# Kernel tuning notes

Measured on AMD Instinct MI355X. Metric: run time of the kernel, lower is better.

The kernel has to match this reference:

```python
import jax, jax.numpy as jnp
import numpy as np

N_LAYERS = 4
EPS = 1e-5  # eqx.nn.LayerNorm default


def _kernels(lam, P, B, C, step, L):
    # Annotated-S4 DPLR generating-function kernel (Q = P), vectorized over H channels.
    # lam, P, B, C: (H, N) complex64; step: (H, 1) real. Returns K: (H, L) real.
    omega = jnp.exp((-2j * jnp.pi) * (jnp.arange(L) / L))            # (L,) roots of unity
    g = (2.0 / step) * ((1.0 - omega) / (1.0 + omega))[None, :]      # (H, L) bilinear warp
    c = 2.0 / (1.0 + omega)                                          # (L,)

    def cauchy(v):  # v: (H, N) -> (H, L): sum_n v_n / (g - lambda_n)
        return jnp.sum(v[:, None, :] / (g[:, :, None] - lam[:, None, :]), axis=-1)

    k00 = cauchy(jnp.conj(C) * B)
    k01 = cauchy(jnp.conj(C) * P)
    k10 = cauchy(jnp.conj(P) * B)
    k11 = cauchy(jnp.conj(P) * P)
    at_roots = c[None, :] * (k00 - k01 * (1.0 / (1.0 + k11)) * k10)  # woodbury correction
    return jnp.fft.ifft(at_roots, n=L, axis=-1).real                 # (H, L)


def _causal_conv(u, K):
    # u: (B, L, H) real input, K: (H, L) real kernel -> causal conv along L via zero-padded FFT.
    L = u.shape[1]
    Ud = jnp.fft.rfft(u, n=2 * L, axis=1)                 # (B, F, H)
    Kd = jnp.fft.rfft(K, n=2 * L, axis=-1)                # (H, F)
    return jnp.fft.irfft(Ud * Kd.T[None], n=2 * L, axis=1)[:, :L]


def _forward(x, enc_w, enc_b, dec_w, dec_b, lam_re, lam_im, p_re, p_im, b_re, b_im,
             c_re, c_im, d, log_step, norm_w, norm_b, w1, b1, w2, b2):
    L = x.shape[1]
    h = x @ enc_w.T + enc_b                               # encoder: (B, L, H)
    for i in range(N_LAYERS):
        skip = h
        mu = h.mean(-1, keepdims=True)
        var = ((h - mu) ** 2).mean(-1, keepdims=True)
        hn = (h - mu) / jnp.sqrt(var + EPS) * norm_w[i] + norm_b[i]
        K = _kernels(lam_re[i] + 1j * lam_im[i], p_re[i] + 1j * p_im[i],
                     b_re[i] + 1j * b_im[i], c_re[i] + 1j * c_im[i],
                     jnp.exp(log_step[i])[:, None], L)
        y = _causal_conv(hn, K) + hn * d[i]               # SSM conv + skip-through D term
        y = jax.nn.gelu(y)
        y = (y @ w1[i].T + b1[i]) * jax.nn.sigmoid(y @ w2[i].T + b2[i])  # gated MLP
        h = skip + y
    return h @ dec_w.T + dec_b                            # decoder: (B, L, out)


def setup_inputs() -> dict:
    key = jax.random.key(0)
    B, L, IN, OUT, H, N, NL = 8, 2048, 64, 64, 128, 64, N_LAYERS
    ks = jax.random.split(key, 12)
    rn = lambda k, s, sc: (jax.random.normal(k, s) * sc).astype(jnp.float32)
    return dict(
        x=rn(ks[0], (B, L, IN), 1.0),
        convolve=1,
        enc_w=rn(ks[1], (H, IN), 1.0 / np.sqrt(IN)), enc_b=jnp.zeros((H,), jnp.float32),
        dec_w=rn(ks[2], (OUT, H), 1.0 / np.sqrt(H)), dec_b=jnp.zeros((OUT,), jnp.float32),
        lam_re=-0.5 * jnp.ones((NL, H, N), jnp.float32),  # HiPPO/S4D-style stable poles
        lam_im=jnp.tile(jnp.float32(np.pi) * jnp.arange(N, dtype=jnp.float32), (NL, H, 1)),
        p_re=rn(ks[3], (NL, H, N), 0.5 / np.sqrt(N)), p_im=rn(ks[4], (NL, H, N), 0.5 / np.sqrt(N)),
        b_re=rn(ks[5], (NL, H, N), 1.0), b_im=rn(ks[6], (NL, H, N), 1.0),
        c_re=rn(ks[7], (NL, H, N), 1.0 / np.sqrt(N)), c_im=rn(ks[8], (NL, H, N), 1.0 / np.sqrt(N)),
        d=jnp.ones((NL, H), jnp.float32),
        log_step=(jax.random.uniform(ks[9], (NL, H)) * (np.log(0.1) - np.log(0.001))
                  + np.log(0.001)).astype(jnp.float32),
        norm_w=jnp.ones((NL, H), jnp.float32), norm_b=jnp.zeros((NL, H), jnp.float32),
        w1=rn(ks[10], (NL, H, H), 1.0 / np.sqrt(H)), b1=jnp.zeros((NL, H), jnp.float32),
        w2=rn(ks[11], (NL, H, H), 1.0 / np.sqrt(H)), b2=jnp.zeros((NL, H), jnp.float32),
    )


def reference(x, convolve, enc_w, enc_b, dec_w, dec_b, lam_re, lam_im, p_re, p_im,
              b_re, b_im, c_re, c_im, d, log_step, norm_w, norm_b, w1, b1, w2, b2):
    # convolve is static 1 (True): the FFT-convolution path of the S4 Model.
    return _forward(x, enc_w, enc_b, dec_w, dec_b, lam_re, lam_im, p_re, p_im, b_re, b_im,
                    c_re, c_im, d, log_step, norm_w, norm_b, w1, b1, w2, b2)
```

## Files before the change

kernel.cpp:

```cpp
#include <hip/hip_runtime.h>
#include <hip/hip_bf16.h>


#define Bsz 8
#define Lseq 2048
#define Hdim 128
#define Npol 64
#define NLAYERS 4

typedef __bf16 bf16x8 __attribute__((ext_vector_type(8)));
typedef float f32x16 __attribute__((ext_vector_type(16)));

__device__ __forceinline__ float fast_rcp(float x) { return __builtin_amdgcn_rcpf(x); }
__device__ __forceinline__ float fast_rsq(float x) { return __builtin_amdgcn_rsqf(x); }

__device__ __forceinline__ float2 cmulf(float2 a, float2 b) {
    return make_float2(a.x * b.x - a.y * b.y, a.x * b.y + a.y * b.x);
}
__device__ __forceinline__ float2 cmulc(float2 a, float2 b) {
    return make_float2(a.x * b.x + a.y * b.y, a.y * b.x - a.x * b.y);
}

__device__ __forceinline__ float gelu_f(float v) {
    float z = 0.7978845608028654f * (v + 0.044715f * v * v * v);
    float e = __expf(2.0f * z);
    return v - v * fast_rcp(e + 1.0f);
}

__device__ __forceinline__ int sw(int i) { return (i & ~15) | ((i ^ (i >> 4)) & 15); }

static __device__ const float W16R[8] = {1.f, 0.9238795325f, 0.7071067812f, 0.3826834324f,
                                         0.f, -0.3826834324f, -0.7071067812f, -0.9238795325f};
static __device__ const float W16I[8] = {0.f, -0.3826834324f, -0.7071067812f, -0.9238795325f,
                                         -1.f, -0.9238795325f, -0.7071067812f, -0.3826834324f};
static __device__ const int BR4[16] = {0, 8, 4, 12, 2, 10, 6, 14, 1, 9, 5, 13, 3, 11, 7, 15};
static __device__ const int BR3[8] = {0, 4, 2, 6, 1, 5, 3, 7};

__device__ __forceinline__ float2 twget(const float2* __restrict__ tw, int e) {
    float2 w = tw[e & 2047];
    if (e & 2048) { w.x = -w.x; w.y = -w.y; }
    return w;
}

template <bool INV>
__device__ __forceinline__ void fft16_dif(float2 v[16]) {
#pragma unroll
    for (int mi = 0; mi < 4; mi++) {
        const int m = 8 >> mi;
#pragma unroll
        for (int g = 0; g < 16; g += 2 * m) {
#pragma unroll
            for (int j = 0; j < m; j++) {
                float wr = W16R[j << mi];
                float wi = INV ? -W16I[j << mi] : W16I[j << mi];
                float2 a = v[g + j], b = v[g + j + m];
                float dx = a.x - b.x, dy = a.y - b.y;
                v[g + j] = make_float2(a.x + b.x, a.y + b.y);
                v[g + j + m] = make_float2(dx * wr - dy * wi, dx * wi + dy * wr);
            }
        }
    }
}

template <bool INV>
__device__ __forceinline__ void fft16_dit(float2 v[16]) {
#pragma unroll
    for (int mi = 3; mi >= 0; mi--) {
        const int m = 8 >> mi;
#pragma unroll
        for (int g = 0; g < 16; g += 2 * m) {
#pragma unroll
            for (int j = 0; j < m; j++) {
                float wr = W16R[j << mi];
                float wi = INV ? -W16I[j << mi] : W16I[j << mi];
                float2 a = v[g + j], b = v[g + j + m];
                float bx = b.x * wr - b.y * wi, by = b.x * wi + b.y * wr;
                v[g + j] = make_float2(a.x + bx, a.y + by);
                v[g + j + m] = make_float2(a.x - bx, a.y - by);
            }
        }
    }
}

template <bool INV>
__device__ __forceinline__ void fft8_dif(float2 v[8]) {
#pragma unroll
    for (int mi = 0; mi < 3; mi++) {
        const int m = 4 >> mi;
#pragma unroll
        for (int g = 0; g < 8; g += 2 * m) {
#pragma unroll
            for (int j = 0; j < m; j++) {
                float wr = W16R[j << (mi + 1)];
                float wi = INV ? -W16I[j << (mi + 1)] : W16I[j << (mi + 1)];
                float2 a = v[g + j], b = v[g + j + m];
                float dx = a.x - b.x, dy = a.y - b.y;
                v[g + j] = make_float2(a.x + b.x, a.y + b.y);
                v[g + j + m] = make_float2(dx * wr - dy * wi, dx * wi + dy * wr);
            }
        }
    }
}

__device__ __forceinline__ void fft4096_passA_hz(float2* data, const float2* __restrict__ tw,
                                                 int t, const float2 vin[8]) {
    float2 v[16];
#pragma unroll
    for (int j = 0; j < 8; j++) v[j] = vin[j];
#pragma unroll
    for (int j = 0; j < 8; j++)
        v[j + 8] = cmulf(v[j], make_float2(W16R[j], W16I[j]));
#pragma unroll
    for (int mi = 1; mi < 4; mi++) {
        const int m = 8 >> mi;
#pragma unroll
        for (int g = 0; g < 16; g += 2 * m) {
#pragma unroll
            for (int j = 0; j < m; j++) {
                float wr = W16R[j << mi], wi = W16I[j << mi];
                float2 a = v[g + j], b = v[g + j + m];
                float dx = a.x - b.x, dy = a.y - b.y;
                v[g + j] = make_float2(a.x + b.x, a.y + b.y);
                v[g + j + m] = make_float2(dx * wr - dy * wi, dx * wi + dy * wr);
            }
        }
    }
#pragma unroll
    for (int i = 1; i < 16; i++) v[i] = cmulf(v[i], twget(tw, t * BR4[i]));
#pragma unroll
    for (int i = 0; i < 16; i++) data[sw(i * 256 + t)] = v[i];
}

__device__ __forceinline__ void fft4096_fwd_BC(float2* data, const float2* __restrict__ tw, int t) {
    __syncthreads();
    {
        int j0 = t & 15;
        int base = (t >> 4) * 256 + j0;
        float2 v[16];
#pragma unroll
        for (int k = 0; k < 16; k++) v[k] = data[sw(base + 16 * k)];
        fft16_dif<false>(v);
#pragma unroll
        for (int i = 1; i < 16; i++) v[i] = cmulf(v[i], twget(tw, 16 * j0 * BR4[i]));
#pragma unroll
        for (int i = 0; i < 16; i++) data[sw(base + 16 * i)] = v[i];
    }
    __syncthreads();
    {
        float2 v[16];
#pragma unroll
        for (int k = 0; k < 16; k++) v[k] = data[sw(t * 16 + k)];
        fft16_dif<false>(v);
#pragma unroll
        for (int i = 0; i < 16; i++) data[sw(t * 16 + i)] = v[i];
    }
    __syncthreads();
}

__global__ __launch_bounds__(256, 4) void prep_kernel(const float* __restrict__ lam_re,
                                                      const float* __restrict__ lam_im,
                                                      const float* __restrict__ p_re,
                                                      const float* __restrict__ p_im,
                                                      const float* __restrict__ b_re,
                                                      const float* __restrict__ b_im,
                                                      const float* __restrict__ c_re,
                                                      const float* __restrict__ c_im,
                                                      const float* __restrict__ log_step,
                                                      const float* __restrict__ w1,
                                                      const float* __restrict__ w2,
                                                      float2* __restrict__ tw,
                                                      __bf16* __restrict__ wbf,
                                                      float2* __restrict__ at_roots) {
    int bid = blockIdx.x, t = threadIdx.x;
    if (bid < 8) {
        int k = bid * 256 + t;
        if (k < 2048) {
            double a = -6.283185307179586476925286766559 * (double)k / 4096.0;
            tw[k] = make_float2((float)cos(a), (float)sin(a));
        }
        return;
    }
    if (bid < 264) {
        int i = (bid - 8) * 256 + t;
        int layer = i >> 14, rem = i & 16383;
        wbf[((size_t)layer * 2) * 16384 + rem] = (__bf16)w1[i];
        wbf[((size_t)layer * 2 + 1) * 16384 + rem] = (__bf16)w2[i];
        return;
    }
    int s = bid - 264;
    int h = s & 127, layer = (s >> 7) & 3;
    int l0 = 512 * (s >> 9);
    __shared__ __align__(16) float4 polA[Npol];
    __shared__ __align__(16) float4 polB[Npol];
    __shared__ float n11S[Npol];
    int baseP = (layer * Hdim + h) * Npol;
    if (t < Npol) {
        int n = t;
        float lr = lam_re[baseP + n], li = lam_im[baseP + n];
        float pr = p_re[baseP + n], pi = p_im[baseP + n];
        float br = b_re[baseP + n], bi = b_im[baseP + n];
        float cr = c_re[baseP + n], ci = c_im[baseP + n];
        polA[n] = make_float4(lr, li, cr * br + ci * bi, cr * bi - ci * br);
        polB[n] = make_float4(cr * pr + ci * pi, cr * pi - ci * pr,
                              pr * br + pi * bi, pr * bi - pi * br);
        n11S[n] = pr * pr + pi * pi;
    }
    __syncthreads();
    float step = expf(log_step[layer * Hdim + h]);
    float gs = 2.0f / step;

    float gr[2], gi[2];
#pragma unroll
    for (int j = 0; j < 2; j++) {
        int l = l0 + t + 256 * j;
        float ang = -6.283185307179586f * (float)l / (float)Lseq;
        float wr = cosf(ang), wi = sinf(ang);
        float dr = 1.0f + wr, di = wi;
        float invd2 = fast_rcp(dr * dr + di * di);
        float nr = 1.0f - wr, ni = -wi;
        gr[j] = gs * (nr * dr + ni * di) * invd2;
        gi[j] = gs * (ni * dr - nr * di) * invd2;
    }
    float k00x[2] = {0, 0}, k00y[2] = {0, 0};
    float k01x[2] = {0, 0}, k01y[2] = {0, 0};
    float k10x[2] = {0, 0}, k10y[2] = {0, 0};
    float k11x[2] = {0, 0}, k11y[2] = {0, 0};
#pragma unroll 4
    for (int n = 0; n < Npol; n++) {
        float4 A = polA[n];
        float4 B = polB[n];
        float n11 = n11S[n];
#pragma unroll
        for (int j = 0; j < 2; j++) {
            float er = gr[j] - A.x, ei = gi[j] - A.y;
            float inv2 = fast_rcp(fmaf(er, er, ei * ei));
            float ir = er * inv2;
            float mi = ei * inv2;
            k00x[j] = fmaf(A.z, ir, fmaf(A.w, mi, k00x[j]));
            k00y[j] = fmaf(A.w, ir, fmaf(-A.z, mi, k00y[j]));
            k01x[j] = fmaf(B.x, ir, fmaf(B.y, mi, k01x[j]));
            k01y[j] = fmaf(B.y, ir, fmaf(-B.x, mi, k01y[j]));
            k10x[j] = fmaf(B.z, ir, fmaf(B.w, mi, k10x[j]));
            k10y[j] = fmaf(B.w, ir, fmaf(-B.z, mi, k10y[j]));
            k11x[j] = fmaf(n11, ir, k11x[j]);
            k11y[j] = fmaf(-n11, mi, k11y[j]);
        }
    }
#pragma unroll
    for (int j = 0; j < 2; j++) {
        int l = l0 + t + 256 * j;
        float ang = -6.283185307179586f * (float)l / (float)Lseq;
        float wr = cosf(ang), wi = sinf(ang);
        float dr = 1.0f + wr, di = wi;
        float invd2 = fast_rcp(dr * dr + di * di);
        float cr2 = 2.0f * dr * invd2, ci2 = -2.0f * di * invd2;
        float wr2 = 1.0f + k11x[j], wi2 = k11y[j];
        float w2inv = fast_rcp(fmaf(wr2, wr2, wi2 * wi2));
        float vr = wr2 * w2inv, vi = -wi2 * w2inv;
        float t1x = k01x[j] * k10x[j] - k01y[j] * k10y[j];
        float t1y = k01x[j] * k10y[j] + k01y[j] * k10x[j];
        float t2x = t1x * vr - t1y * vi, t2y = t1x * vi + t1y * vr;
        float ex = k00x[j] - t2x, ey = k00y[j] - t2y;
        at_roots[((size_t)layer * Hdim + h) * Lseq + l] =
            make_float2(cr2 * ex - ci2 * ey, cr2 * ey + ci2 * ex);
    }
}

__global__ __launch_bounds__(256) void kfft_enc_kernel(const float2* __restrict__ at_roots,
                                                       float2* __restrict__ Kd1,
                                                       const float2* __restrict__ tw,
                                                       const float* __restrict__ x,
                                                       const float* __restrict__ enc_w,
                                                       const float* __restrict__ enc_b,
                                                       const float* __restrict__ nw,
                                                       const float* __restrict__ nb,
                                                       float* __restrict__ h,
                                                       float* __restrict__ hnT) {
    __shared__ __align__(16) float smem[11712];
    int bid = blockIdx.x, t = threadIdx.x;
    if (bid < 512) {
        int hh = bid & 127, layer = bid >> 7;
        float2* data = (float2*)smem;
        float* ktmp = smem + 8192;
        const float2* src = at_roots + ((size_t)layer * Hdim + hh) * Lseq;
#pragma unroll
        for (int k = 0; k < 8; k++) {
            int l = t + 256 * k;
            data[sw(l)] = src[l];
        }
        __syncthreads();
        if (t < 128) {
            float2 v[16];
#pragma unroll
            for (int k = 0; k < 16; k++) v[k] = data[sw(t + 128 * k)];
            fft16_dif<true>(v);
#pragma unroll
            for (int i = 1; i < 16; i++) v[i] = cmulc(v[i], twget(tw, 2 * t * BR4[i]));
#pragma unroll
            for (int i = 0; i < 16; i++) data[sw(i * 128 + t)] = v[i];
        }
        __syncthreads();
        if (t < 128) {
            int i2 = t >> 3, j0 = t & 7;
            int base2 = i2 * 128 + j0;
            float2 v[16];
#pragma unroll
            for (int k = 0; k < 16; k++) v[k] = data[sw(base2 + 8 * k)];
            fft16_dif<true>(v);
#pragma unroll
            for (int i = 1; i < 16; i++) v[i] = cmulc(v[i], twget(tw, 32 * j0 * BR4[i]));
#pragma unroll
            for (int i = 0; i < 16; i++) data[sw(base2 + 8 * i)] = v[i];
        }
        __syncthreads();
        {
            float2 v8[8];
#pragma unroll
            for (int k = 0; k < 8; k++) v8[k] = data[sw(t * 8 + k)];
            fft8_dif<true>(v8);
            int r = BR4[t >> 4], s = BR4[t & 15];
#pragma unroll
            for (int i = 0; i < 8; i++) {
                int l = r + 16 * s + 256 * BR3[i];
                ktmp[l] = v8[i].x * (1.0f / 2048.0f);
            }
        }
        __syncthreads();
        {
            float2 vin[8];
#pragma unroll
            for (int k = 0; k < 8; k++) vin[k] = make_float2(ktmp[t + 256 * k], 0.f);
            fft4096_passA_hz(data, tw, t, vin);
        }
        fft4096_fwd_BC(data, tw, t);
        float2* dst = Kd1 + ((size_t)layer * Hdim + hh) * 4096;
#pragma unroll
        for (int k = 0; k < 16; k++) {
            int p = t + 256 * k;
            dst[p] = data[sw(p)];
        }
    } else {
        int r0 = (bid - 512) * 16;
        float* ws = smem;
        float* xst = smem + 8320;
        float* dots = smem + 9600;
        float2* mv = (float2*)(smem + 11648);
        for (int i = t; i < 128 * 64; i += 256) ws[(i >> 6) * 65 + (i & 63)] = enc_w[i];
        for (int i = t; i < 16 * 64; i += 256) {
            int r = i >> 6, k = i & 63;
            xst[k * 20 + r] = x[(size_t)(r0 + r) * 64 + k];
        }
        __syncthreads();
        int o = t & 127, half = t >> 7;
        float acc[8];
        float bo = enc_b[o];
#pragma unroll
        for (int j = 0; j < 8; j++) acc[j] = bo;
        for (int k = 0; k < 64; k++) {
            float wv = ws[o * 65 + k];
            float4 xa = *(const float4*)&xst[k * 20 + half * 8];
            float4 xb = *(const float4*)&xst[k * 20 + half * 8 + 4];
            acc[0] += wv * xa.x; acc[1] += wv * xa.y; acc[2] += wv * xa.z; acc[3] += wv * xa.w;
            acc[4] += wv * xb.x; acc[5] += wv * xb.y; acc[6] += wv * xb.z; acc[7] += wv * xb.w;
        }
#pragma unroll
        for (int j = 0; j < 8; j++) dots[(half * 8 + j) * 128 + o] = acc[j];
        __syncthreads();
        {
            int row = t >> 4, lane = t & 15;
            float s1 = 0.f, s2 = 0.f;
#pragma unroll
            for (int i = 0; i < 8; i++) {
                float v = dots[row * 128 + lane * 8 + i];
                s1 += v; s2 += v * v;
            }
#pragma unroll
            for (int m = 1; m < 16; m <<= 1) { s1 += __shfl_xor(s1, m); s2 += __shfl_xor(s2, m); }
            if (lane == 0) {
                float mu = s1 * (1.0f / 128.0f);
                float var = s2 * (1.0f / 128.0f) - mu * mu;
                mv[row] = make_float2(mu, fast_rsq(var + 1e-5f));
            }
        }
        __syncthreads();
        int c = t & 127;
        int bb = r0 >> 11, l0 = r0 & 2047;
        float nwc = nw[c], nbc = nb[c];
        float hnv[8];
#pragma unroll
        for (int j = 0; j < 8; j++) {
            int r = half * 8 + j;
            float v = dots[r * 128 + c];
            h[(size_t)(r0 + r) * Hdim + c] = v;
            float2 m = mv[r];
            hnv[j] = (v - m.x) * m.y * nwc + nbc;
        }
        float* dst = hnT + ((size_t)bb * Hdim + c) * Lseq + l0 + half * 8;
        *(float4*)dst = make_float4(hnv[0], hnv[1], hnv[2], hnv[3]);
        *(float4*)(dst + 4) = make_float4(hnv[4], hnv[5], hnv[6], hnv[7]);
    }
}

__global__ __launch_bounds__(256) void conv_kernel(float* __restrict__ hnT,
                                                   const float2* __restrict__ Kd1,
                                                   const float* __restrict__ dvec,
                                                   const float2* __restrict__ tw) {
    int h = blockIdx.x, bp = blockIdx.y, t = threadIdx.x;
    __shared__ float2 data[4096];
    float* u0 = hnT + ((size_t)(2 * bp) * Hdim + h) * Lseq;
    float* u1 = hnT + ((size_t)(2 * bp + 1) * Hdim + h) * Lseq;
    float2 ureg[8];
    {
        float2 vin[8];
#pragma unroll
        for (int k = 0; k < 8; k++) {
            int l = t + 256 * k;
            float2 u2 = make_float2(u0[l], u1[l]);
            ureg[k] = u2;
            vin[k] = u2;
        }
        fft4096_passA_hz(data, tw, t, vin);
    }
    fft4096_fwd_BC(data, tw, t);
    const float2* Kp = Kd1 + (size_t)h * 4096;
    const float scale = 1.0f / 4096.0f;
#pragma unroll
    for (int k = 0; k < 16; k++) {
        int p = t + 256 * k;
        float2 Z = data[sw(p)];
        float2 Kv = Kp[p];
        float2 W = cmulf(Z, Kv);
        data[sw(p)] = make_float2(W.x * scale, W.y * scale);
    }
    __syncthreads();
    {
        float2 v[16];
#pragma unroll
        for (int i = 0; i < 16; i++) v[i] = data[sw(t * 16 + i)];
        fft16_dit<true>(v);
#pragma unroll
        for (int i = 0; i < 16; i++) data[sw(t * 16 + i)] = v[i];
    }
    __syncthreads();
    {
        int j0 = t & 15;
        int base2 = (t >> 4) * 256 + j0;
        float2 v[16];
        v[0] = data[sw(base2)];
#pragma unroll
        for (int i = 1; i < 16; i++)
            v[i] = cmulc(data[sw(base2 + 16 * i)], twget(tw, 16 * j0 * BR4[i]));
        fft16_dit<true>(v);
#pragma unroll
        for (int i = 0; i < 16; i++) data[sw(base2 + 16 * i)] = v[i];
    }
    __syncthreads();
    {
        float2 v[16];
        v[0] = data[sw(t)];
#pragma unroll
        for (int i = 1; i < 16; i++)
            v[i] = cmulc(data[sw(i * 256 + t)], twget(tw, t * BR4[i]));
#pragma unroll
        for (int mi = 3; mi >= 1; mi--) {
            const int m = 8 >> mi;
#pragma unroll
            for (int g = 0; g < 16; g += 2 * m) {
#pragma unroll
                for (int j = 0; j < m; j++) {
                    float wr = W16R[j << mi], wi = -W16I[j << mi];
                    float2 a = v[g + j], bb2 = v[g + j + m];
                    float bx = bb2.x * wr - bb2.y * wi, by = bb2.x * wi + bb2.y * wr;
                    v[g + j] = make_float2(a.x + bx, a.y + by);
                    v[g + j + m] = make_float2(a.x - bx, a.y - by);
                }
            }
        }
#pragma unroll
        for (int j = 0; j < 8; j++) {
            float wr = W16R[j], wi = -W16I[j];
            float2 bb2 = v[j + 8];
            float bx = bb2.x * wr - bb2.y * wi, by = bb2.x * wi + bb2.y * wr;
            v[j] = make_float2(v[j].x + bx, v[j].y + by);
        }
        float dcoef = dvec[h];
#pragma unroll
        for (int k = 0; k < 8; k++) {
            int l = t + 256 * k;
            u0[l] = gelu_f(v[k].x + ureg[k].x * dcoef);
            u1[l] = gelu_f(v[k].y + ureg[k].y * dcoef);
        }
    }
}

__global__ __launch_bounds__(256) void mlp_kernel(const float* __restrict__ yT,
                                                  float* __restrict__ h,
                                                  float* __restrict__ hnT,
                                                  const __bf16* __restrict__ w1b,
                                                  const __bf16* __restrict__ w2b,
                                                  const float* __restrict__ b1,
                                                  const float* __restrict__ b2,
                                                  const float* __restrict__ nw,
                                                  const float* __restrict__ nb,
                                                  int do_ln) {
    int r0 = blockIdx.x * 32;
    int t = threadIdx.x;
    int wave = t >> 6, lane = t & 63;
    __shared__ __align__(16) __bf16 ybf[32 * 136];
    __shared__ float dots[32 * 132];
    __shared__ float2 mv[32];
    int bb = r0 >> 11, l0 = r0 & 2047;
    for (int i = t; i < 32 * 128; i += 256) {
        int r = i & 31, k = i >> 5;
        ybf[r * 136 + k] = (__bf16)yT[((size_t)bb * Hdim + k) * Lseq + l0 + r];
    }
    __syncthreads();
    int m = lane & 31, half = lane >> 5;
    bf16x8 a[8];
#pragma unroll
    for (int kk = 0; kk < 8; kk++)
        a[kk] = *(const bf16x8*)&ybf[m * 136 + kk * 16 + half * 8];
    int out = 32 * wave + m;
    const __bf16* w1r = w1b + (size_t)out * 128 + half * 8;
    const __bf16* w2r = w2b + (size_t)out * 128 + half * 8;
    f32x16 acc1, acc2;
#pragma unroll
    for (int i = 0; i < 16; i++) { acc1[i] = 0.f; acc2[i] = 0.f; }
#pragma unroll
    for (int kk = 0; kk < 8; kk++) {
        bf16x8 bw1 = *(const bf16x8*)(w1r + kk * 16);
        bf16x8 bw2 = *(const bf16x8*)(w2r + kk * 16);
        acc1 = __builtin_amdgcn_mfma_f32_32x32x16_bf16(a[kk], bw1, acc1, 0, 0, 0);
        acc2 = __builtin_amdgcn_mfma_f32_32x32x16_bf16(a[kk], bw2, acc2, 0, 0, 0);
    }
    float bias1 = b1[out], bias2 = b2[out];
#pragma unroll
    for (int reg = 0; reg < 16; reg++) {
        int row = (reg & 3) + 8 * (reg >> 2) + 4 * half;
        float v1 = acc1[reg] + bias1;
        float v2 = acc2[reg] + bias2;
        float g = fast_rcp(1.0f + __expf(-v2));
        float hv = h[(size_t)(r0 + row) * Hdim + out] + v1 * g;
        dots[row * 132 + out] = hv;
    }
    __syncthreads();
    if (do_ln) {
        int row = t >> 3, lane8 = t & 7;
        float s1 = 0.f, s2 = 0.f;
        int base = row * 132 + lane8 * 16;
#pragma unroll
        for (int q = 0; q < 4; q++) {
            float4 v4 = *(const float4*)&dots[base + 4 * q];
            s1 += v4.x + v4.y + v4.z + v4.w;
            s2 += v4.x * v4.x + v4.y * v4.y + v4.z * v4.z + v4.w * v4.w;
        }
#pragma unroll
        for (int mm = 1; mm < 8; mm <<= 1) { s1 += __shfl_xor(s1, mm); s2 += __shfl_xor(s2, mm); }
        if (lane8 == 0) {
            float mu = s1 * (1.0f / 128.0f);
            float var = s2 * (1.0f / 128.0f) - mu * mu;
            mv[row] = make_float2(mu, fast_rsq(var + 1e-5f));
        }
        __syncthreads();
        int o = t & 127, rh = t >> 7;
        float nwc = nw[o], nbc = nb[o];
        float hnv[16];
#pragma unroll
        for (int j = 0; j < 16; j++) {
            int r = rh * 16 + j;
            float hvv = dots[r * 132 + o];
            h[(size_t)(r0 + r) * Hdim + o] = hvv;
            float2 mvv = mv[r];
            hnv[j] = (hvv - mvv.x) * mvv.y * nwc + nbc;
        }
        float* dst = hnT + ((size_t)bb * Hdim + o) * Lseq + l0 + rh * 16;
        *(float4*)(dst)      = make_float4(hnv[0],  hnv[1],  hnv[2],  hnv[3]);
        *(float4*)(dst + 4)  = make_float4(hnv[4],  hnv[5],  hnv[6],  hnv[7]);
        *(float4*)(dst + 8)  = make_float4(hnv[8],  hnv[9],  hnv[10], hnv[11]);
        *(float4*)(dst + 12) = make_float4(hnv[12], hnv[13], hnv[14], hnv[15]);
    } else {
        int o = t & 127, rh = t >> 7;
#pragma unroll
        for (int j = 0; j < 16; j++) {
            int r = rh * 16 + j;
            h[(size_t)(r0 + r) * Hdim + o] = dots[r * 132 + o];
        }
    }
}

__global__ __launch_bounds__(256) void decoder_kernel(const float* __restrict__ h,
                                                      const float* __restrict__ w,
                                                      const float* __restrict__ b,
                                                      float* __restrict__ out) {
    int r0 = blockIdx.x * 32;
    int t = threadIdx.x;
    __shared__ float ws[64 * 129];
    __shared__ __align__(16) float hst[128 * 36];
    for (int i = t; i < 64 * 128; i += 256) ws[(i >> 7) * 129 + (i & 127)] = w[i];
    for (int i = t; i < 32 * 128; i += 256) {
        int r = i >> 7, k = i & 127;
        hst[k * 36 + r] = h[(size_t)(r0 + r) * Hdim + k];
    }
    __syncthreads();
    int o = t & 63, q = t >> 6;
    float acc[8];
    float bo = b[o];
#pragma unroll
    for (int j = 0; j < 8; j++) acc[j] = bo;
    for (int k = 0; k < 128; k++) {
        float wv = ws[o * 129 + k];
        float4 ha = *(const float4*)&hst[k * 36 + q * 8];
        float4 hb = *(const float4*)&hst[k * 36 + q * 8 + 4];
        acc[0] += wv * ha.x; acc[1] += wv * ha.y; acc[2] += wv * ha.z; acc[3] += wv * ha.w;
        acc[4] += wv * hb.x; acc[5] += wv * hb.y; acc[6] += wv * hb.z; acc[7] += wv * hb.w;
    }
#pragma unroll
    for (int j = 0; j < 8; j++) out[(size_t)(r0 + q * 8 + j) * 64 + o] = acc[j];
}

extern "C" void kernel_launch(void* const* d_in, const int* in_sizes, int n_in,
                              void* d_out, int out_size, void* d_ws, size_t ws_size,
                              hipStream_t stream) {
    const float* x      = (const float*)d_in[0];
    const float* enc_w  = (const float*)d_in[2];
    const float* enc_b  = (const float*)d_in[3];
    const float* dec_w  = (const float*)d_in[4];
    const float* dec_b  = (const float*)d_in[5];
    const float* lam_re = (const float*)d_in[6];
    const float* lam_im = (const float*)d_in[7];
    const float* p_re   = (const float*)d_in[8];
    const float* p_im   = (const float*)d_in[9];
    const float* b_re   = (const float*)d_in[10];
    const float* b_im   = (const float*)d_in[11];
    const float* c_re   = (const float*)d_in[12];
    const float* c_im   = (const float*)d_in[13];
    const float* dvec   = (const float*)d_in[14];
    const float* lstep  = (const float*)d_in[15];
    const float* norm_w = (const float*)d_in[16];
    const float* norm_b = (const float*)d_in[17];
    const float* w1     = (const float*)d_in[18];
    const float* b1     = (const float*)d_in[19];
    const float* w2     = (const float*)d_in[20];
    const float* b2     = (const float*)d_in[21];
    float* out = (float*)d_out;

    char* ws = (char*)d_ws;
    float2* tw  = (float2*)ws;  ws += 2048 * sizeof(float2);
    float*  h   = (float*)ws;   ws += (size_t)Bsz * Lseq * Hdim * sizeof(float);
    float*  hnT = (float*)ws;   ws += (size_t)Bsz * Lseq * Hdim * sizeof(float);
    float2* atr = (float2*)ws;  ws += (size_t)NLAYERS * Hdim * Lseq * sizeof(float2);
    float2* Kd1 = (float2*)ws;  ws += (size_t)NLAYERS * Hdim * 4096 * sizeof(float2);
    __bf16* wbf = (__bf16*)ws;  ws += (size_t)NLAYERS * 2 * Hdim * Hdim * sizeof(__bf16);

    const int nrows = Bsz * Lseq;

    prep_kernel<<<8 + 256 + 2048, 256, 0, stream>>>(
        lam_re, lam_im, p_re, p_im, b_re, b_im, c_re, c_im, lstep, w1, w2, tw, wbf, atr);
    kfft_enc_kernel<<<512 + nrows / 16, 256, 0, stream>>>(
        atr, Kd1, tw, x, enc_w, enc_b, norm_w, norm_b, h, hnT);
    for (int L = 0; L < NLAYERS; L++) {
        conv_kernel<<<dim3(Hdim, Bsz / 2), 256, 0, stream>>>(
            hnT, Kd1 + (size_t)L * Hdim * 4096, dvec + L * Hdim, tw);
        int do_ln = (L < NLAYERS - 1) ? 1 : 0;
        const float* nwn = norm_w + ((L + 1) % NLAYERS) * Hdim;
        const float* nbn = norm_b + ((L + 1) % NLAYERS) * Hdim;
        const __bf16* w1bL = wbf + (size_t)L * 2 * Hdim * Hdim;
        const __bf16* w2bL = w1bL + Hdim * Hdim;
        mlp_kernel<<<nrows / 32, 256, 0, stream>>>(hnT, h, hnT, w1bL, w2bL,
                                                   b1 + L * Hdim, b2 + L * Hdim,
                                                   nwn, nbn, do_ln);
    }
    decoder_kernel<<<nrows / 32, 256, 0, stream>>>(h, dec_w, dec_b, out);
}
```

Baseline: 310.3 us.

## Fuse final MLP with bf16 MFMA decoder and prefetch conv kernel spectrum

The last layer's gated MLP is merged with the decoder into one kernel. The updated h stays in shared memory and is projected to the outputs with bf16 MFMA, using decoder weights converted in the prep kernel. This removes the final h write and reread plus one launch, at the cost of bf16 rounding in the decoder, which used to run in fp32. Separately, the conv kernel loads its frequency-domain filter into registers before the forward FFT so that load latency overlaps the transform, which adds register pressure.

```diff
diff --git a/kernel.cpp b/kernel.cpp
--- a/kernel.cpp
+++ b/kernel.cpp
@@ -168,8 +168,10 @@
                                                       const float* __restrict__ log_step,
                                                       const float* __restrict__ w1,
                                                       const float* __restrict__ w2,
+                                                      const float* __restrict__ dec_w,
                                                       float2* __restrict__ tw,
                                                       __bf16* __restrict__ wbf,
+                                                      __bf16* __restrict__ decbf,
                                                       float2* __restrict__ at_roots) {
     int bid = blockIdx.x, t = threadIdx.x;
     if (bid < 8) {
@@ -187,7 +189,12 @@
         wbf[((size_t)layer * 2 + 1) * 16384 + rem] = (__bf16)w2[i];
         return;
     }
-    int s = bid - 264;
+    if (bid < 296) {
+        int i = (bid - 264) * 256 + t;
+        decbf[i] = (__bf16)dec_w[i];
+        return;
+    }
+    int s = bid - 296;
     int h = s & 127, layer = (s >> 7) & 3;
     int l0 = 512 * (s >> 9);
     __shared__ __align__(16) float4 polA[Npol];
@@ -410,6 +417,8 @@
     float* u0 = hnT + ((size_t)(2 * bp) * Hdim + h) * Lseq;
     float* u1 = hnT + ((size_t)(2 * bp + 1) * Hdim + h) * Lseq;
     float2 ureg[8];
+    float2 Kreg[16];
+    const float2* Kp = Kd1 + (size_t)h * 4096;
     {
         float2 vin[8];
 #pragma unroll
@@ -419,17 +428,17 @@
             ureg[k] = u2;
             vin[k] = u2;
         }
+#pragma unroll
+        for (int k = 0; k < 16; k++) Kreg[k] = Kp[t + 256 * k];
         fft4096_passA_hz(data, tw, t, vin);
     }
     fft4096_fwd_BC(data, tw, t);
-    const float2* Kp = Kd1 + (size_t)h * 4096;
     const float scale = 1.0f / 4096.0f;
 #pragma unroll
     for (int k = 0; k < 16; k++) {
         int p = t + 256 * k;
         float2 Z = data[sw(p)];
-        float2 Kv = Kp[p];
-        float2 W = cmulf(Z, Kv);
+        float2 W = cmulf(Z, Kreg[k]);
         data[sw(p)] = make_float2(W.x * scale, W.y * scale);
     }
     __syncthreads();
@@ -501,8 +510,7 @@
                                                   const float* __restrict__ b1,
                                                   const float* __restrict__ b2,
                                                   const float* __restrict__ nw,
-                                                  const float* __restrict__ nb,
-                                                  int do_ln) {
+                                                  const float* __restrict__ nb) {
     int r0 = blockIdx.x * 32;
     int t = threadIdx.x;
     int wave = t >> 6, lane = t & 63;
@@ -544,7 +552,7 @@
         dots[row * 132 + out] = hv;
     }
     __syncthreads();
-    if (do_ln) {
+    {
         int row = t >> 3, lane8 = t & 7;
         float s1 = 0.f, s2 = 0.f;
         int base = row * 132 + lane8 * 16;
@@ -561,7 +569,9 @@
             float var = s2 * (1.0f / 128.0f) - mu * mu;
             mv[row] = make_float2(mu, fast_rsq(var + 1e-5f));
         }
-        __syncthreads();
+    }
+    __syncthreads();
+    {
         int o = t & 127, rh = t >> 7;
         float nwc = nw[o], nbc = nb[o];
         float hnv[16];
@@ -578,44 +588,85 @@
         *(float4*)(dst + 4)  = make_float4(hnv[4],  hnv[5],  hnv[6],  hnv[7]);
         *(float4*)(dst + 8)  = make_float4(hnv[8],  hnv[9],  hnv[10], hnv[11]);
         *(float4*)(dst + 12) = make_float4(hnv[12], hnv[13], hnv[14], hnv[15]);
-    } else {
-        int o = t & 127, rh = t >> 7;
-#pragma unroll
-        for (int j = 0; j < 16; j++) {
-            int r = rh * 16 + j;
-            h[(size_t)(r0 + r) * Hdim + o] = dots[r * 132 + o];
-        }
-    }
-}
-
-__global__ __launch_bounds__(256) void decoder_kernel(const float* __restrict__ h,
-                                                      const float* __restrict__ w,
-                                                      const float* __restrict__ b,
-                                                      float* __restrict__ out) {
+    }
+}
+
+__global__ __launch_bounds__(256) void mlpdec_kernel(const float* __restrict__ yT,
+                                                     const float* __restrict__ h,
+                                                     const __bf16* __restrict__ w1b,
+                                                     const __bf16* __restrict__ w2b,
+                                                     const float* __restrict__ b1,
+                                                     const float* __restrict__ b2,
+                                                     const __bf16* __restrict__ decb,
+                                                     const float* __restrict__ dec_bias,
+                                                     float* __restrict__ out) {
     int r0 = blockIdx.x * 32;
     int t = threadIdx.x;
-    __shared__ float ws[64 * 129];
-    __shared__ __align__(16) float hst[128 * 36];
-    for (int i = t; i < 64 * 128; i += 256) ws[(i >> 7) * 129 + (i & 127)] = w[i];
+    int wave = t >> 6, lane = t & 63;
+    __shared__ __align__(16) __bf16 ybf[32 * 136];
+    __shared__ float dots[32 * 132];
+    int bb = r0 >> 11, l0 = r0 & 2047;
+    for (int i = t; i < 32 * 128; i += 256) {
+        int r = i & 31, k = i >> 5;
+        ybf[r * 136 + k] = (__bf16)yT[((size_t)bb * Hdim + k) * Lseq + l0 + r];
+    }
+    __syncthreads();
+    int m = lane & 31, half = lane >> 5;
+    bf16x8 a[8];
+#pragma unroll
+    for (int kk = 0; kk < 8; kk++)
+        a[kk] = *(const bf16x8*)&ybf[m * 136 + kk * 16 + half * 8];
+    int outc = 32 * wave + m;
+    const __bf16* w1r = w1b + (size_t)outc * 128 + half * 8;
+    const __bf16* w2r = w2b + (size_t)outc * 128 + half * 8;
+    f32x16 acc1, acc2;
+#pragma unroll
+    for (int i = 0; i < 16; i++) { acc1[i] = 0.f; acc2[i] = 0.f; }
+#pragma unroll
+    for (int kk = 0; kk < 8; kk++) {
+        bf16x8 bw1 = *(const bf16x8*)(w1r + kk * 16);
+        bf16x8 bw2 = *(const bf16x8*)(w2r + kk * 16);
+        acc1 = __builtin_amdgcn_mfma_f32_32x32x16_bf16(a[kk], bw1, acc1, 0, 0, 0);
+        acc2 = __builtin_amdgcn_mfma_f32_32x32x16_bf16(a[kk], bw2, acc2, 0, 0, 0);
+    }
+    float bias1 = b1[outc], bias2 = b2[outc];
+#pragma unroll
+    for (int reg = 0; reg < 16; reg++) {
+        int row = (reg & 3) + 8 * (reg >> 2) + 4 * half;
+        float v1 = acc1[reg] + bias1;
+        float v2 = acc2[reg] + bias2;
+        float g = fast_rcp(1.0f + __expf(-v2));
+        float hv = h[(size_t)(r0 + row) * Hdim + outc] + v1 * g;
+        dots[row * 132 + outc] = hv;
+    }
+    __syncthreads();
     for (int i = t; i < 32 * 128; i += 256) {
         int r = i >> 7, k = i & 127;
-        hst[k * 36 + r] = h[(size_t)(r0 + r) * Hdim + k];
-    }
-    __syncthreads();
-    int o = t & 63, q = t >> 6;
-    float acc[8];
-    float bo = b[o];
-#pragma unroll
-    for (int j = 0; j < 8; j++) acc[j] = bo;
-    for (int k = 0; k < 128; k++) {
-        float wv = ws[o * 129 + k];
-        float4 ha = *(const float4*)&hst[k * 36 + q * 8];
-        float4 hb = *(const float4*)&hst[k * 36 + q * 8 + 4];
-        acc[0] += wv * ha.x; acc[1] += wv * ha.y; acc[2] += wv * ha.z; acc[3] += wv * ha.w;
-        acc[4] += wv * hb.x; acc[5] += wv * hb.y; acc[6] += wv * hb.z; acc[7] += wv * hb.w;
-    }
-#pragma unroll
-    for (int j = 0; j < 8; j++) out[(size_t)(r0 + q * 8 + j) * 64 + o] = acc[j];
+        ybf[r * 136 + k] = (__bf16)dots[r * 132 + k];
+    }
+    __syncthreads();
+    if (wave < 2) {
+        bf16x8 a2[8];
+#pragma unroll
+        for (int kk = 0; kk < 8; kk++)
+            a2[kk] = *(const bf16x8*)&ybf[m * 136 + kk * 16 + half * 8];
+        int oc = 32 * wave + m;
+        const __bf16* wr = decb + (size_t)oc * 128 + half * 8;
+        f32x16 acc;
+#pragma unroll
+        for (int i = 0; i < 16; i++) acc[i] = 0.f;
+#pragma unroll
+        for (int kk = 0; kk < 8; kk++) {
+            bf16x8 bw = *(const bf16x8*)(wr + kk * 16);
+            acc = __builtin_amdgcn_mfma_f32_32x32x16_bf16(a2[kk], bw, acc, 0, 0, 0);
+        }
+        float bo = dec_bias[oc];
+#pragma unroll
+        for (int reg = 0; reg < 16; reg++) {
+            int row = (reg & 3) + 8 * (reg >> 2) + 4 * half;
+            out[(size_t)(r0 + row) * 64 + oc] = acc[reg] + bo;
+        }
+    }
 }
 
 extern "C" void kernel_launch(void* const* d_in, const int* in_sizes, int n_in,
@@ -651,24 +702,30 @@
     float2* atr = (float2*)ws;  ws += (size_t)NLAYERS * Hdim * Lseq * sizeof(float2);
     float2* Kd1 = (float2*)ws;  ws += (size_t)NLAYERS * Hdim * 4096 * sizeof(float2);
     __bf16* wbf = (__bf16*)ws;  ws += (size_t)NLAYERS * 2 * Hdim * Hdim * sizeof(__bf16);
+    __bf16* dbf = (__bf16*)ws;  ws += (size_t)64 * Hdim * sizeof(__bf16);
 
     const int nrows = Bsz * Lseq;
 
-    prep_kernel<<<8 + 256 + 2048, 256, 0, stream>>>(
-        lam_re, lam_im, p_re, p_im, b_re, b_im, c_re, c_im, lstep, w1, w2, tw, wbf, atr);
+    prep_kernel<<<296 + 2048, 256, 0, stream>>>(
+        lam_re, lam_im, p_re, p_im, b_re, b_im, c_re, c_im, lstep, w1, w2, dec_w,
+        tw, wbf, dbf, atr);
     kfft_enc_kernel<<<512 + nrows / 16, 256, 0, stream>>>(
         atr, Kd1, tw, x, enc_w, enc_b, norm_w, norm_b, h, hnT);
     for (int L = 0; L < NLAYERS; L++) {
         conv_kernel<<<dim3(Hdim, Bsz / 2), 256, 0, stream>>>(
             hnT, Kd1 + (size_t)L * Hdim * 4096, dvec + L * Hdim, tw);
-        int do_ln = (L < NLAYERS - 1) ? 1 : 0;
-        const float* nwn = norm_w + ((L + 1) % NLAYERS) * Hdim;
-        const float* nbn = norm_b + ((L + 1) % NLAYERS) * Hdim;
         const __bf16* w1bL = wbf + (size_t)L * 2 * Hdim * Hdim;
         const __bf16* w2bL = w1bL + Hdim * Hdim;
-        mlp_kernel<<<nrows / 32, 256, 0, stream>>>(hnT, h, hnT, w1bL, w2bL,
-                                                   b1 + L * Hdim, b2 + L * Hdim,
-                                                   nwn, nbn, do_ln);
-    }
-    decoder_kernel<<<nrows / 32, 256, 0, stream>>>(h, dec_w, dec_b, out);
-}
+        if (L < NLAYERS - 1) {
+            const float* nwn = norm_w + (L + 1) * Hdim;
+            const float* nbn = norm_b + (L + 1) * Hdim;
+            mlp_kernel<<<nrows / 32, 256, 0, stream>>>(hnT, h, hnT, w1bL, w2bL,
+                                                       b1 + L * Hdim, b2 + L * Hdim,
+                                                       nwn, nbn);
+        } else {
+            mlpdec_kernel<<<nrows / 32, 256, 0, stream>>>(hnT, h, w1bL, w2bL,
+                                                          b1 + L * Hdim, b2 + L * Hdim,
+                                                          dbf, dec_b, out);
+        }
+    }
+}
```

Result: faster. 292.9 us (-5.6%).
